# Optimization experiments

Hardware: AMD Instinct MI355X
Metric: run time of the kernel (lower is better)

The kernel has to match this reference:

```python
import jax, jax.numpy as jnp
import numpy as np

N, L, DV, EF = 64, 128, 16, 4
D, H, FF, LC, K, MS = 256, 8, 1024, 3, 6, 16
DK = D // H
NEG = -1e9


def _ln(x, g, b):
    m = x.mean(-1, keepdims=True)
    v = ((x - m) ** 2).mean(-1, keepdims=True)
    return (x - m) / jnp.sqrt(v + 1e-5) * g + b


def setup_inputs() -> dict:
    key = jax.random.key(0)
    ks = jax.random.split(key, 20)
    s = 0.05
    rn = lambda k, sh: jax.random.normal(k, sh, jnp.float32) * s
    return {
        "vehicles": jax.random.normal(ks[0], (N, L, DV), jnp.float32),
        "fleet_edges": jax.random.uniform(ks[1], (N, L, L, EF), jnp.float32),
        "Wproj": rn(ks[2], (DV, D)), "bproj": jnp.zeros((D,), jnp.float32),
        "Wq": rn(ks[3], (LC, D, D)), "Wk": rn(ks[4], (LC, D, D)), "Wv": rn(ks[5], (LC, D, D)),
        "mix1_w": rn(ks[6], (LC, H, 2, MS)), "mix1_b": jnp.zeros((LC, H, MS), jnp.float32),
        "mix2_w": rn(ks[7], (LC, H, MS)), "mix2_b": jnp.zeros((LC, H), jnp.float32),
        "Wo": rn(ks[8], (LC, D, D)), "bo": jnp.zeros((LC, D), jnp.float32),
        "n1_g": jnp.ones((LC, D), jnp.float32), "n1_b": jnp.zeros((LC, D), jnp.float32),
        "ff1_w": rn(ks[9], (LC, D, FF)), "ff1_b": jnp.zeros((LC, FF), jnp.float32),
        "ff2_w": rn(ks[10], (LC, FF, D)), "ff2_b": jnp.zeros((LC, D), jnp.float32),
        "n2_g": jnp.ones((LC, D), jnp.float32), "n2_b": jnp.zeros((LC, D), jnp.float32),
    }


def _forward(vehicles, fleet_edges, Wproj, bproj, Wq, Wk, Wv, mix1_w, mix1_b,
             mix2_w, mix2_b, Wo, bo, n1_g, n1_b, ff1_w, ff1_b, ff2_w, ff2_b, n2_g, n2_b):
    h = vehicles @ Wproj + bproj                      # (N, L, D)
    dist = fleet_edges[..., 0]                        # (N, L, L)
    cost = dist
    # kNN mask: keep K smallest distances per row; mask==True -> blocked
    _, knn_idx = jax.lax.top_k(-dist, K)              # (N, L, K)
    nbr = jnp.any(jax.nn.one_hot(knn_idx, L, dtype=bool), axis=2)  # (N, L, L)
    mask = ~nbr
    row_fully_masked = mask.all(-1)                   # (N, L)
    inv_sqrt_dk = 1.0 / np.sqrt(DK).astype(np.float32)
    for i in range(LC):
        q = (h @ Wq[i]).reshape(N, L, H, DK).transpose(0, 2, 1, 3)
        k_ = (h @ Wk[i]).reshape(N, L, H, DK).transpose(0, 2, 1, 3)
        v = (h @ Wv[i]).reshape(N, L, H, DK).transpose(0, 2, 1, 3)
        dot = jnp.einsum('nhrd,nhcd->nhrc', q, k_) * inv_sqrt_dk      # (N,H,L,L)
        cost_b = jnp.broadcast_to(cost[:, None], (N, H, L, L))
        two = jnp.stack([dot, cost_b], axis=-1)                        # (N,H,L,L,2)
        ms1 = jax.nn.relu(jnp.einsum('nhrct,htm->nhrcm', two, mix1_w[i])
                          + mix1_b[i][None, :, None, None, :])         # (N,H,L,L,MS)
        score = jnp.einsum('nhrcm,hm->nhrc', ms1, mix2_w[i]) \
                + mix2_b[i][None, :, None, None]                       # (N,H,L,L)
        score = jnp.where(mask[:, None], NEG, score)
        w = jax.nn.softmax(score, axis=-1)
        att = jnp.einsum('nhrc,nhcd->nhrd', w, v)
        att = att.transpose(0, 2, 1, 3).reshape(N, L, D) @ Wo[i] + bo[i]
        h1 = _ln(h + att, n1_g[i], n1_b[i])
        ff = jax.nn.relu(h1 @ ff1_w[i] + ff1_b[i]) @ ff2_w[i] + ff2_b[i]
        h = _ln(h1 + ff, n2_g[i], n2_b[i])
        # original does h_out[mask] = 0; with kNN k>0 every row keeps k entries,
        # so only fully-masked rows would be zeroed (a no-op here, kept for fidelity)
        h = jnp.where(row_fully_masked[..., None], 0.0, h)
    return h


def reference(vehicles, fleet_edges, Wproj, bproj, Wq, Wk, Wv, mix1_w, mix1_b,
              mix2_w, mix2_b, Wo, bo, n1_g, n1_b, ff1_w, ff1_b, ff2_w, ff2_b, n2_g, n2_b):
    return _forward(vehicles, fleet_edges, Wproj, bproj, Wq, Wk, Wv, mix1_w, mix1_b,
                    mix2_w, mix2_b, Wo, bo, n1_g, n1_b, ff1_w, ff1_b, ff2_w, ff2_b, n2_g, n2_b)
```

## Files before the change

kernel.cpp:

```cpp
#include <hip/hip_runtime.h>
#include <math.h>

#define NB 64
#define LL 128
#define DV 16
#define DD 256
#define HH 8
#define DK 32
#define FF 1024
#define LC 3
#define KNN 6
#define MS 16
#define WLS 786432

typedef __attribute__((ext_vector_type(8))) short s16x8;
typedef __attribute__((ext_vector_type(4))) float f32x4;

static __device__ inline unsigned short f2b(float x) {
    union { float f; unsigned int u; } v; v.f = x;
    unsigned int r = (v.u + 0x7FFFu + ((v.u >> 16) & 1u)) >> 16;
    return (unsigned short)r;
}

static __device__ __forceinline__ void glds16(const void* g, void* l) {
    __builtin_amdgcn_global_load_lds(
        (const __attribute__((address_space(1))) void*)g,
        (__attribute__((address_space(3))) void*)l, 16, 0, 0);
}

__global__ __launch_bounds__(256)
void uber_pre(const float* __restrict__ veh, const float* __restrict__ Wp,
              const float* __restrict__ bp, float* __restrict__ h,
              unsigned short* __restrict__ hb,
              const float* __restrict__ edges, unsigned long long* __restrict__ idx8,
              const float* __restrict__ Wq, const float* __restrict__ Wk,
              const float* __restrict__ Wv, const float* __restrict__ Wo,
              const float* __restrict__ f1, const float* __restrict__ f2,
              unsigned short* __restrict__ Wt) {
    int bx = blockIdx.x;
    if (bx < 2048) {
        int m = bx * 4 + (threadIdx.x >> 6);
        int l = threadIdx.x & 63;
        int c0 = l * 4;
        const float4* w4 = reinterpret_cast<const float4*>(Wp);
        float4 a = *reinterpret_cast<const float4*>(bp + c0);
        const float* vr = veh + (size_t)m * DV;
#pragma unroll
        for (int t = 0; t < DV; ++t) {
            float vt = vr[t];
            float4 wv = w4[t * 64 + l];
            a.x += vt * wv.x; a.y += vt * wv.y; a.z += vt * wv.z; a.w += vt * wv.w;
        }
        *reinterpret_cast<float4*>(h + (size_t)m * DD + c0) = a;
        ushort4 u; u.x = f2b(a.x); u.y = f2b(a.y); u.z = f2b(a.z); u.w = f2b(a.w);
        *reinterpret_cast<ushort4*>(hb + (size_t)m * DD + c0) = u;
        return;
    }
    if (bx < 4096) {
        int row = (bx - 2048) * 4 + (threadIdx.x >> 6);
        int lane = threadIdx.x & 63;
        const float* dr = edges + (size_t)row * LL * 4;
        float v0 = dr[lane * 4], v1 = dr[(lane + 64) * 4];
        int i0 = lane, i1 = lane + 64;
        unsigned long long packed = 0;
#pragma unroll
        for (int k = 0; k < KNN; ++k) {
            float v; int i;
            if (v1 < v0) { v = v1; i = i1; } else { v = v0; i = i0; }
#pragma unroll
            for (int o = 1; o < 64; o <<= 1) {
                float ov = __shfl_xor(v, o);
                int oi = __shfl_xor(i, o);
                if (ov < v || (ov == v && oi < i)) { v = ov; i = oi; }
            }
            packed |= (unsigned long long)i << (k * 8);
            if (i == i0) v0 = 3.4e38f;
            if (i == i1) v1 = 3.4e38f;
        }
        if (lane == 0) idx8[row] = packed;
        return;
    }
    {
        int t = bx - 4096;
        int ll = t / 768, r = t % 768;
        int w, tile, K, N;
        if (r < 256)      { w = r >> 6; tile = r & 63;  K = DD; N = DD; }
        else if (r < 512) { w = 4; tile = r - 256;      K = DD; N = FF; }
        else              { w = 5; tile = r - 512;      K = FF; N = DD; }
        const float* src = (w == 0) ? Wq : (w == 1) ? Wk : (w == 2) ? Wv :
                           (w == 3) ? Wo : (w == 4) ? f1 : f2;
        src += (size_t)ll * K * N;
        long off = (w == 4) ? 262144L : (w == 5) ? 524288L : (long)w * 65536L;
        unsigned short* dst = Wt + (size_t)ll * WLS + off;
        int ntx = N >> 5;
        int n0 = (tile % ntx) * 32, k0 = (tile / ntx) * 32;
        int tx = threadIdx.x & 31, ty = threadIdx.x >> 5;
        __shared__ float T[32][33];
#pragma unroll
        for (int rr = 0; rr < 4; ++rr)
            T[ty + rr * 8][tx] = src[(size_t)(k0 + ty + rr * 8) * N + n0 + tx];
        __syncthreads();
#pragma unroll
        for (int rr = 0; rr < 4; ++rr)
            dst[(size_t)(n0 + ty + rr * 8) * K + k0 + tx] = f2b(T[tx][ty + rr * 8]);
    }
}

template <int BM, int BN, int WR, int WC, int MODE>
__global__ __launch_bounds__(256)
void gg(const unsigned short* __restrict__ A, const unsigned short* __restrict__ Bt,
        const float* __restrict__ bias, unsigned short* __restrict__ Cb,
        float* __restrict__ Oq, float* __restrict__ Ok, float* __restrict__ Ov,
        int K, int N) {
    constexpr int MI = BM / (WR * 16);
    constexpr int NJ = BN / (WC * 16);
    __shared__ unsigned short As[BM * 32];
    __shared__ unsigned short Bs[BN * 32];
    int tid = threadIdx.x;
    int w = tid >> 6, l = tid & 63;
    int lr = l & 15, lg = l >> 4;
    int wr = w % WR, wc = w / WR;
    int m0 = blockIdx.y * BM, n0 = blockIdx.x * BN;
    int row = tid >> 2, seg = tid & 3;

    f32x4 acc[MI][NJ];
#pragma unroll
    for (int i = 0; i < MI; ++i)
#pragma unroll
        for (int j = 0; j < NJ; ++j) acc[i][j] = (f32x4)(0.f);

    for (int k0 = 0; k0 < K; k0 += 32) {
        __syncthreads();
#pragma unroll
        for (int r = 0; r < BM / 64; ++r)
            glds16(A + (size_t)(m0 + r * 64 + row) * K + k0 + seg * 8,
                   As + r * 2048 + w * 512);
#pragma unroll
        for (int r = 0; r < BN / 64; ++r)
            glds16(Bt + (size_t)(n0 + r * 64 + row) * K + k0 + seg * 8,
                   Bs + r * 2048 + w * 512);
        __syncthreads();
        s16x8 af[MI], bf[NJ];
#pragma unroll
        for (int i = 0; i < MI; ++i)
            af[i] = *reinterpret_cast<const s16x8*>(
                As + (wr * MI * 16 + i * 16 + lr) * 32 + lg * 8);
#pragma unroll
        for (int j = 0; j < NJ; ++j)
            bf[j] = *reinterpret_cast<const s16x8*>(
                Bs + (wc * NJ * 16 + j * 16 + lr) * 32 + lg * 8);
#pragma unroll
        for (int i = 0; i < MI; ++i)
#pragma unroll
            for (int j = 0; j < NJ; ++j)
                acc[i][j] = __builtin_amdgcn_mfma_f32_16x16x32_bf16(af[i], bf[j], acc[i][j], 0, 0, 0);
    }

    if constexpr (MODE == 2) {
        int s = n0 >> 8;
        int nn = blockIdx.y;
        float* dst = (s == 0) ? Oq : (s == 1) ? Ok : Ov;
#pragma unroll
        for (int i = 0; i < MI; ++i)
#pragma unroll
            for (int j = 0; j < NJ; ++j) {
                int cc = (n0 & 255) + j * 16 + lr;
                int hh = cc >> 5, dk = cc & 31;
                int rl = wr * MI * 16 + i * 16 + lg * 4;
                size_t ho = ((size_t)(nn * HH + hh) * LL + rl) * DK + dk;
#pragma unroll
                for (int q = 0; q < 4; ++q)
                    dst[ho + (size_t)q * DK] = acc[i][j][q];
            }
    } else {
#pragma unroll
        for (int i = 0; i < MI; ++i)
#pragma unroll
            for (int j = 0; j < NJ; ++j) {
                int col = n0 + wc * NJ * 16 + j * 16 + lr;
                float bc = bias[col];
#pragma unroll
                for (int q = 0; q < 4; ++q) {
                    int r = m0 + wr * MI * 16 + i * 16 + lg * 4 + q;
                    float v = fmaxf(acc[i][j][q] + bc, 0.f);
                    Cb[(size_t)r * N + col] = f2b(v);
                }
            }
    }
}

template <int KK>
__global__ __launch_bounds__(256)
void gg_ln(const unsigned short* __restrict__ A, const unsigned short* __restrict__ Bt,
           const float* __restrict__ bias, const float* __restrict__ res,
           const float* __restrict__ g, const float* __restrict__ be,
           float* __restrict__ out, unsigned short* __restrict__ outb) {
    __shared__ unsigned short As[16 * 32];
    __shared__ unsigned short Bs[256 * 32];
    __shared__ float Red[16][4];
    int tid = threadIdx.x;
    int w = tid >> 6, l = tid & 63;
    int lr = l & 15, lg = l >> 4;
    int m0 = blockIdx.x * 16;

    f32x4 acc[4];
#pragma unroll
    for (int j = 0; j < 4; ++j) acc[j] = (f32x4)(0.f);

    for (int k0 = 0; k0 < KK; k0 += 32) {
        __syncthreads();
        if (w == 0)
            glds16(A + (size_t)(m0 + (l >> 2)) * KK + k0 + (l & 3) * 8, As);
#pragma unroll
        for (int i = 0; i < 4; ++i) {
            int idx = w * 4 + i;
            glds16(Bt + (size_t)(idx * 16 + (l >> 2)) * KK + k0 + (l & 3) * 8,
                   Bs + idx * 512);
        }
        __syncthreads();
        s16x8 af = *reinterpret_cast<const s16x8*>(As + lr * 32 + lg * 8);
#pragma unroll
        for (int j = 0; j < 4; ++j) {
            s16x8 bf = *reinterpret_cast<const s16x8*>(
                Bs + (w * 64 + j * 16 + lr) * 32 + lg * 8);
            acc[j] = __builtin_amdgcn_mfma_f32_16x16x32_bf16(af, bf, acc[j], 0, 0, 0);
        }
    }

    float rsum[4] = {0.f, 0.f, 0.f, 0.f};
#pragma unroll
    for (int j = 0; j < 4; ++j) {
        int col = w * 64 + j * 16 + lr;
        float bc = bias[col];
#pragma unroll
        for (int q = 0; q < 4; ++q) {
            float x = acc[j][q] + bc + res[(size_t)(m0 + lg * 4 + q) * DD + col];
            acc[j][q] = x;
            rsum[q] += x;
        }
    }
#pragma unroll
    for (int q = 0; q < 4; ++q)
#pragma unroll
        for (int o = 1; o < 16; o <<= 1) rsum[q] += __shfl_xor(rsum[q], o);
    __syncthreads();
    if (lr == 0)
#pragma unroll
        for (int q = 0; q < 4; ++q) Red[lg * 4 + q][w] = rsum[q];
    __syncthreads();
    float mean[4];
#pragma unroll
    for (int q = 0; q < 4; ++q) {
        int row = lg * 4 + q;
        mean[q] = (Red[row][0] + Red[row][1] + Red[row][2] + Red[row][3]) * (1.0f / 256.0f);
    }
    float ssum[4] = {0.f, 0.f, 0.f, 0.f};
#pragma unroll
    for (int j = 0; j < 4; ++j)
#pragma unroll
        for (int q = 0; q < 4; ++q) {
            float d = acc[j][q] - mean[q];
            ssum[q] += d * d;
        }
#pragma unroll
    for (int q = 0; q < 4; ++q)
#pragma unroll
        for (int o = 1; o < 16; o <<= 1) ssum[q] += __shfl_xor(ssum[q], o);
    __syncthreads();
    if (lr == 0)
#pragma unroll
        for (int q = 0; q < 4; ++q) Red[lg * 4 + q][w] = ssum[q];
    __syncthreads();
    float rstd[4];
#pragma unroll
    for (int q = 0; q < 4; ++q) {
        int row = lg * 4 + q;
        float var = (Red[row][0] + Red[row][1] + Red[row][2] + Red[row][3]) * (1.0f / 256.0f);
        rstd[q] = 1.0f / sqrtf(var + 1e-5f);
    }
#pragma unroll
    for (int j = 0; j < 4; ++j) {
        int col = w * 64 + j * 16 + lr;
        float gc = g[col], bc2 = be[col];
#pragma unroll
        for (int q = 0; q < 4; ++q) {
            size_t off = (size_t)(m0 + lg * 4 + q) * DD + col;
            float v = (acc[j][q] - mean[q]) * rstd[q] * gc + bc2;
            out[off] = v;
            outb[off] = f2b(v);
        }
    }
}

__global__ __launch_bounds__(256)
void fattn7(const float* __restrict__ qh, const float* __restrict__ kh,
            const float* __restrict__ vh, const float* __restrict__ edges,
            const unsigned long long* __restrict__ idx8,
            const float* __restrict__ m1w, const float* __restrict__ m1b,
            const float* __restrict__ m2w, const float* __restrict__ m2b,
            unsigned short* __restrict__ attc) {
    int t = blockIdx.x * 256 + threadIdx.x;
    int bh = t >> 7, r = t & 127;
    int n = bh >> 3, hh = bh & 7;
    int hu = __builtin_amdgcn_readfirstlane(hh);
    const float* w0g = m1w + (hu * 2 + 0) * MS;
    const float* w1g = m1w + (hu * 2 + 1) * MS;
    const float* b1g = m1b + hu * MS;
    const float* w2g = m2w + hu * MS;
    float b2v = m2b[hu];
    const float scale = 0.17677669529663687f;

    const float4* qr = reinterpret_cast<const float4*>(qh + ((size_t)bh * LL + r) * DK);
    float4 q[8];
#pragma unroll
    for (int j = 0; j < 8; ++j) q[j] = qr[j];

    unsigned long long pk = idx8[(size_t)n * LL + r];
    const float* kbase = kh + (size_t)bh * LL * DK;
    const float* vbase = vh + (size_t)bh * LL * DK;
    const float* erow = edges + (size_t)(n * LL + r) * LL * 4;

    int col[KNN];
#pragma unroll
    for (int k = 0; k < KNN; ++k) col[k] = (int)((pk >> (k * 8)) & 0xFF);

    float e[KNN];
    float mx = -3.4e38f;
#pragma unroll
    for (int k = 0; k < KNN; ++k) {
        const float4* kr = reinterpret_cast<const float4*>(kbase + (size_t)col[k] * DK);
        float d = 0.f;
#pragma unroll
        for (int j = 0; j < 8; ++j) {
            float4 kv = kr[j];
            d += q[j].x * kv.x + q[j].y * kv.y + q[j].z * kv.z + q[j].w * kv.w;
        }
        d *= scale;
        float cst = erow[col[k] * 4];
        float s = b2v;
#pragma unroll
        for (int m = 0; m < MS; ++m)
            s += fmaxf(d * w0g[m] + cst * w1g[m] + b1g[m], 0.f) * w2g[m];
        e[k] = s;
        mx = fmaxf(mx, s);
    }
    float sum = 0.f;
#pragma unroll
    for (int k = 0; k < KNN; ++k) { e[k] = __expf(e[k] - mx); sum += e[k]; }
    float inv = 1.f / sum;

    float4 att[8];
#pragma unroll
    for (int j = 0; j < 8; ++j) att[j] = make_float4(0.f, 0.f, 0.f, 0.f);
#pragma unroll
    for (int k = 0; k < KNN; ++k) {
        float wgt = e[k] * inv;
        const float4* vr = reinterpret_cast<const float4*>(vbase + (size_t)col[k] * DK);
#pragma unroll
        for (int j = 0; j < 8; ++j) {
            float4 vv = vr[j];
            att[j].x += wgt * vv.x; att[j].y += wgt * vv.y;
            att[j].z += wgt * vv.z; att[j].w += wgt * vv.w;
        }
    }
    unsigned short* dst = attc + ((size_t)(n * LL + r)) * DD + hh * DK;
#pragma unroll
    for (int j = 0; j < 8; ++j) {
        ushort4 u;
        u.x = f2b(att[j].x); u.y = f2b(att[j].y);
        u.z = f2b(att[j].z); u.w = f2b(att[j].w);
        *reinterpret_cast<ushort4*>(dst + j * 4) = u;
    }
}

extern "C" void kernel_launch(void* const* d_in, const int* in_sizes, int n_in,
                              void* d_out, int out_size, void* d_ws, size_t ws_size,
                              hipStream_t stream) {
    const float* vehicles = (const float*)d_in[0];
    const float* fleet    = (const float*)d_in[1];
    const float* Wproj    = (const float*)d_in[2];
    const float* bproj    = (const float*)d_in[3];
    const float* Wq       = (const float*)d_in[4];
    const float* Wk       = (const float*)d_in[5];
    const float* Wv       = (const float*)d_in[6];
    const float* m1w      = (const float*)d_in[7];
    const float* m1b      = (const float*)d_in[8];
    const float* m2w      = (const float*)d_in[9];
    const float* m2b      = (const float*)d_in[10];
    const float* Wo       = (const float*)d_in[11];
    const float* bo       = (const float*)d_in[12];
    const float* n1_g     = (const float*)d_in[13];
    const float* n1_b     = (const float*)d_in[14];
    const float* ff1_w    = (const float*)d_in[15];
    const float* ff1_b    = (const float*)d_in[16];
    const float* ff2_w    = (const float*)d_in[17];
    const float* ff2_b    = (const float*)d_in[18];
    const float* n2_g     = (const float*)d_in[19];
    const float* n2_b     = (const float*)d_in[20];

    const size_t MROWS = (size_t)NB * LL;
    const size_t HSZ   = MROWS * DD;

    float* ws = (float*)d_ws;
    float* h   = ws;
    float* qh  = h + HSZ;
    float* kh  = qh + HSZ;
    float* vh  = kh + HSZ;
    unsigned short* hb    = (unsigned short*)(vh + HSZ);
    unsigned short* attc  = hb + HSZ;
    unsigned short* ffmid = attc + HSZ;
    unsigned short* Wt    = ffmid + MROWS * FF;
    unsigned long long* idx8 = (unsigned long long*)(Wt + 3 * WLS);

    uber_pre<<<6400, 256, 0, stream>>>(vehicles, Wproj, bproj, h, hb,
                                       fleet, idx8,
                                       Wq, Wk, Wv, Wo, ff1_w, ff2_w, Wt);

    dim3 gqkv(12, 64);
    dim3 gff1(8, 64);

    for (int i = 0; i < LC; ++i) {
        const unsigned short* wt = Wt + (size_t)i * WLS;

        gg<128, 64, 4, 1, 2><<<gqkv, 256, 0, stream>>>(
            hb, wt, nullptr, nullptr, qh, kh, vh, DD, 768);

        fattn7<<<256, 256, 0, stream>>>(
            qh, kh, vh, fleet, idx8,
            m1w + (size_t)i * HH * 2 * MS, m1b + (size_t)i * HH * MS,
            m2w + (size_t)i * HH * MS,     m2b + (size_t)i * HH,
            attc);

        gg_ln<256><<<512, 256, 0, stream>>>(
            attc, wt + 196608, bo + (size_t)i * DD,
            h, n1_g + (size_t)i * DD, n1_b + (size_t)i * DD, h, hb);

        gg<128, 128, 2, 2, 1><<<gff1, 256, 0, stream>>>(
            hb, wt + 262144, ff1_b + (size_t)i * FF, ffmid,
            nullptr, nullptr, nullptr, DD, FF);

        float* dst = (i == LC - 1) ? (float*)d_out : h;
        gg_ln<1024><<<512, 256, 0, stream>>>(
            ffmid, wt + 524288, ff2_b + (size_t)i * DD,
            h, n2_g + (size_t)i * DD, n2_b + (size_t)i * DD, dst, hb);
    }
}
```

Baseline: 247.5 us.

## Fuse sparse kNN attention into the Wo projection + LayerNorm kernel

Removes the separate attention kernel and computes the kNN-masked attention rows directly inside the Wo GEMM+LayerNorm block. The bf16 attention output now goes into shared memory instead of a global buffer, with two threads per (row, head) splitting the head dimension and combining dot products via a shuffle. This cuts one launch per layer and the global write/read of the attention buffer. In exchange the block does the attention work up front before its GEMM loop starts, and it uses more shared memory for the padded A tile.

```diff
diff --git a/kernel.cpp b/kernel.cpp
--- a/kernel.cpp
+++ b/kernel.cpp
@@ -189,13 +189,19 @@
     }
 }
 
-template <int KK>
+template <int KK, bool ATT>
 __global__ __launch_bounds__(256)
 void gg_ln(const unsigned short* __restrict__ A, const unsigned short* __restrict__ Bt,
+           const float* __restrict__ qh, const float* __restrict__ kh,
+           const float* __restrict__ vh, const float* __restrict__ edges,
+           const unsigned long long* __restrict__ idx8,
+           const float* __restrict__ m1w, const float* __restrict__ m1b,
+           const float* __restrict__ m2w, const float* __restrict__ m2b,
            const float* __restrict__ bias, const float* __restrict__ res,
            const float* __restrict__ g, const float* __restrict__ be,
            float* __restrict__ out, unsigned short* __restrict__ outb) {
-    __shared__ unsigned short As[16 * 32];
+    constexpr int ASTRIDE = ATT ? 264 : 32;
+    __shared__ unsigned short As[16 * ASTRIDE];
     __shared__ unsigned short Bs[256 * 32];
     __shared__ float Red[16][4];
     int tid = threadIdx.x;
@@ -203,14 +209,95 @@
     int lr = l & 15, lg = l >> 4;
     int m0 = blockIdx.x * 16;
 
+    if constexpr (ATT) {
+        int task = tid >> 1, sub = tid & 1;
+        int rl = task & 15, hh = task >> 4;
+        int n = m0 >> 7, r = (m0 & 127) + rl;
+        int bh = n * HH + hh;
+        const float scale = 0.17677669529663687f;
+        const float* w0g = m1w + (hh * 2 + 0) * MS;
+        const float* w1g = m1w + (hh * 2 + 1) * MS;
+        const float* b1g = m1b + hh * MS;
+        const float* w2g = m2w + hh * MS;
+        float b2v = m2b[hh];
+
+        const float4* qr = reinterpret_cast<const float4*>(
+            qh + ((size_t)bh * LL + r) * DK) + sub * 4;
+        float4 q[4];
+#pragma unroll
+        for (int j = 0; j < 4; ++j) q[j] = qr[j];
+
+        unsigned long long pk = idx8[(size_t)n * LL + r];
+        const float* kbase = kh + (size_t)bh * LL * DK;
+        const float* vbase = vh + (size_t)bh * LL * DK;
+        const float* erow = edges + (size_t)(n * LL + r) * LL * 4;
+
+        int col[KNN];
+#pragma unroll
+        for (int k = 0; k < KNN; ++k) col[k] = (int)((pk >> (k * 8)) & 0xFF);
+
+        float e[KNN];
+        float mx = -3.4e38f;
+#pragma unroll
+        for (int k = 0; k < KNN; ++k) {
+            const float4* kr = reinterpret_cast<const float4*>(
+                kbase + (size_t)col[k] * DK) + sub * 4;
+            float d = 0.f;
+#pragma unroll
+            for (int j = 0; j < 4; ++j) {
+                float4 kv = kr[j];
+                d += q[j].x * kv.x + q[j].y * kv.y + q[j].z * kv.z + q[j].w * kv.w;
+            }
+            d += __shfl_xor(d, 1);
+            d *= scale;
+            float cst = erow[col[k] * 4];
+            float s = b2v;
+#pragma unroll
+            for (int m = 0; m < MS; ++m)
+                s += fmaxf(d * w0g[m] + cst * w1g[m] + b1g[m], 0.f) * w2g[m];
+            e[k] = s;
+            mx = fmaxf(mx, s);
+        }
+        float sum = 0.f;
+#pragma unroll
+        for (int k = 0; k < KNN; ++k) { e[k] = __expf(e[k] - mx); sum += e[k]; }
+        float inv = 1.f / sum;
+
+        float4 att[4];
+#pragma unroll
+        for (int j = 0; j < 4; ++j) att[j] = make_float4(0.f, 0.f, 0.f, 0.f);
+#pragma unroll
+        for (int k = 0; k < KNN; ++k) {
+            float wgt = e[k] * inv;
+            const float4* vr = reinterpret_cast<const float4*>(
+                vbase + (size_t)col[k] * DK) + sub * 4;
+#pragma unroll
+            for (int j = 0; j < 4; ++j) {
+                float4 vv = vr[j];
+                att[j].x += wgt * vv.x; att[j].y += wgt * vv.y;
+                att[j].z += wgt * vv.z; att[j].w += wgt * vv.w;
+            }
+        }
+        unsigned short* arow = As + rl * ASTRIDE + hh * DK + sub * 16;
+#pragma unroll
+        for (int j = 0; j < 4; ++j) {
+            ushort4 u;
+            u.x = f2b(att[j].x); u.y = f2b(att[j].y);
+            u.z = f2b(att[j].z); u.w = f2b(att[j].w);
+            *reinterpret_cast<ushort4*>(arow + j * 4) = u;
+        }
+    }
+
     f32x4 acc[4];
 #pragma unroll
     for (int j = 0; j < 4; ++j) acc[j] = (f32x4)(0.f);
 
     for (int k0 = 0; k0 < KK; k0 += 32) {
         __syncthreads();
-        if (w == 0)
-            glds16(A + (size_t)(m0 + (l >> 2)) * KK + k0 + (l & 3) * 8, As);
+        if constexpr (!ATT) {
+            if (w == 0)
+                glds16(A + (size_t)(m0 + (l >> 2)) * KK + k0 + (l & 3) * 8, As);
+        }
 #pragma unroll
         for (int i = 0; i < 4; ++i) {
             int idx = w * 4 + i;
@@ -218,7 +305,11 @@
                    Bs + idx * 512);
         }
         __syncthreads();
-        s16x8 af = *reinterpret_cast<const s16x8*>(As + lr * 32 + lg * 8);
+        s16x8 af;
+        if constexpr (ATT)
+            af = *reinterpret_cast<const s16x8*>(As + lr * ASTRIDE + k0 + lg * 8);
+        else
+            af = *reinterpret_cast<const s16x8*>(As + lr * ASTRIDE + lg * 8);
 #pragma unroll
         for (int j = 0; j < 4; ++j) {
             s16x8 bf = *reinterpret_cast<const s16x8*>(
@@ -289,87 +380,6 @@
             out[off] = v;
             outb[off] = f2b(v);
         }
-    }
-}
-
-__global__ __launch_bounds__(256)
-void fattn7(const float* __restrict__ qh, const float* __restrict__ kh,
-            const float* __restrict__ vh, const float* __restrict__ edges,
-            const unsigned long long* __restrict__ idx8,
-            const float* __restrict__ m1w, const float* __restrict__ m1b,
-            const float* __restrict__ m2w, const float* __restrict__ m2b,
-            unsigned short* __restrict__ attc) {
-    int t = blockIdx.x * 256 + threadIdx.x;
-    int bh = t >> 7, r = t & 127;
-    int n = bh >> 3, hh = bh & 7;
-    int hu = __builtin_amdgcn_readfirstlane(hh);
-    const float* w0g = m1w + (hu * 2 + 0) * MS;
-    const float* w1g = m1w + (hu * 2 + 1) * MS;
-    const float* b1g = m1b + hu * MS;
-    const float* w2g = m2w + hu * MS;
-    float b2v = m2b[hu];
-    const float scale = 0.17677669529663687f;
-
-    const float4* qr = reinterpret_cast<const float4*>(qh + ((size_t)bh * LL + r) * DK);
-    float4 q[8];
-#pragma unroll
-    for (int j = 0; j < 8; ++j) q[j] = qr[j];
-
-    unsigned long long pk = idx8[(size_t)n * LL + r];
-    const float* kbase = kh + (size_t)bh * LL * DK;
-    const float* vbase = vh + (size_t)bh * LL * DK;
-    const float* erow = edges + (size_t)(n * LL + r) * LL * 4;
-
-    int col[KNN];
-#pragma unroll
-    for (int k = 0; k < KNN; ++k) col[k] = (int)((pk >> (k * 8)) & 0xFF);
-
-    float e[KNN];
-    float mx = -3.4e38f;
-#pragma unroll
-    for (int k = 0; k < KNN; ++k) {
-        const float4* kr = reinterpret_cast<const float4*>(kbase + (size_t)col[k] * DK);
-        float d = 0.f;
-#pragma unroll
-        for (int j = 0; j < 8; ++j) {
-            float4 kv = kr[j];
-            d += q[j].x * kv.x + q[j].y * kv.y + q[j].z * kv.z + q[j].w * kv.w;
-        }
-        d *= scale;
-        float cst = erow[col[k] * 4];
-        float s = b2v;
-#pragma unroll
-        for (int m = 0; m < MS; ++m)
-            s += fmaxf(d * w0g[m] + cst * w1g[m] + b1g[m], 0.f) * w2g[m];
-        e[k] = s;
-        mx = fmaxf(mx, s);
-    }
-    float sum = 0.f;
-#pragma unroll
-    for (int k = 0; k < KNN; ++k) { e[k] = __expf(e[k] - mx); sum += e[k]; }
-    float inv = 1.f / sum;
-
-    float4 att[8];
-#pragma unroll
-    for (int j = 0; j < 8; ++j) att[j] = make_float4(0.f, 0.f, 0.f, 0.f);
-#pragma unroll
-    for (int k = 0; k < KNN; ++k) {
-        float wgt = e[k] * inv;
-        const float4* vr = reinterpret_cast<const float4*>(vbase + (size_t)col[k] * DK);
-#pragma unroll
-        for (int j = 0; j < 8; ++j) {
-            float4 vv = vr[j];
-            att[j].x += wgt * vv.x; att[j].y += wgt * vv.y;
-            att[j].z += wgt * vv.z; att[j].w += wgt * vv.w;
-        }
-    }
-    unsigned short* dst = attc + ((size_t)(n * LL + r)) * DD + hh * DK;
-#pragma unroll
-    for (int j = 0; j < 8; ++j) {
-        ushort4 u;
-        u.x = f2b(att[j].x); u.y = f2b(att[j].y);
-        u.z = f2b(att[j].z); u.w = f2b(att[j].w);
-        *reinterpret_cast<ushort4*>(dst + j * 4) = u;
     }
 }
 
@@ -407,8 +417,7 @@
     float* kh  = qh + HSZ;
     float* vh  = kh + HSZ;
     unsigned short* hb    = (unsigned short*)(vh + HSZ);
-    unsigned short* attc  = hb + HSZ;
-    unsigned short* ffmid = attc + HSZ;
+    unsigned short* ffmid = hb + HSZ;
     unsigned short* Wt    = ffmid + MROWS * FF;
     unsigned long long* idx8 = (unsigned long long*)(Wt + 3 * WLS);
 
@@ -425,14 +434,12 @@
         gg<128, 64, 4, 1, 2><<<gqkv, 256, 0, stream>>>(
             hb, wt, nullptr, nullptr, qh, kh, vh, DD, 768);
 
-        fattn7<<<256, 256, 0, stream>>>(
+        gg_ln<256, true><<<512, 256, 0, stream>>>(
+            nullptr, wt + 196608,
             qh, kh, vh, fleet, idx8,
             m1w + (size_t)i * HH * 2 * MS, m1b + (size_t)i * HH * MS,
             m2w + (size_t)i * HH * MS,     m2b + (size_t)i * HH,
-            attc);
-
-        gg_ln<256><<<512, 256, 0, stream>>>(
-            attc, wt + 196608, bo + (size_t)i * DD,
+            bo + (size_t)i * DD,
             h, n1_g + (size_t)i * DD, n1_b + (size_t)i * DD, h, hb);
 
         gg<128, 128, 2, 2, 1><<<gff1, 256, 0, stream>>>(
@@ -440,8 +447,11 @@
             nullptr, nullptr, nullptr, DD, FF);
 
         float* dst = (i == LC - 1) ? (float*)d_out : h;
-        gg_ln<1024><<<512, 256, 0, stream>>>(
-            ffmid, wt + 524288, ff2_b + (size_t)i * DD,
+        gg_ln<1024, false><<<512, 256, 0, stream>>>(
+            ffmid, wt + 524288,
+            nullptr, nullptr, nullptr, nullptr, nullptr,
+            nullptr, nullptr, nullptr, nullptr,
+            ff2_b + (size_t)i * DD,
             h, n2_g + (size_t)i * DD, n2_b + (size_t)i * DD, dst, hb);
     }
 }
```

Measured after the change: 240.1 us. -3.0%, faster.
